# Kernel optimization log

Hardware: AMD Instinct MI355X
Metric: run time of the kernel (lower is better)

Reference implementation:

```python
import jax, jax.numpy as jnp
import numpy as np

BN_EPS = 1e-5

def knn_indices(loc, new_loc, k):
    # squared distances [B, M, N] via ||y||^2 + ||x||^2 - 2 y.x (no [B,M,N,3] materialization)
    x2 = jnp.sum(loc * loc, axis=-1)          # [B, N]
    y2 = jnp.sum(new_loc * new_loc, axis=-1)  # [B, M]
    d2 = y2[:, :, None] + x2[:, None, :] - 2.0 * jnp.einsum('bmc,bnc->bmn', new_loc, loc)
    _, idx = jax.lax.top_k(-d2, k)            # smallest-k -> [B, M, K]
    return idx

def gather_neighbors(x, idx):
    # x [B, N, C], idx [B, M, K] -> [B, M, K, C]
    return jax.vmap(lambda xb, ib: xb[ib])(x, idx)

def conv_bn_relu(x, W, g, b):
    # x [B, Cin, M, K]; 1x1 conv (no bias) + training-mode BatchNorm2d + ReLU
    y = jnp.einsum('oc,bcmk->bomk', W, x)
    mu = jnp.mean(y, axis=(0, 2, 3), keepdims=True)
    var = jnp.var(y, axis=(0, 2, 3), keepdims=True)  # biased, as torch BN uses for normalization
    y = (y - mu) * jax.lax.rsqrt(var + BN_EPS)
    return jax.nn.relu(y * g[None, :, None, None] + b[None, :, None, None])

def setup_inputs() -> dict:
    key = jax.random.key(0)
    ks = jax.random.split(key, 8)
    B, N, M, C = 16, 4096, 1024, 64
    loc = jax.random.normal(ks[0], (B, N, 3), dtype=jnp.float32)
    new_loc = jax.random.normal(ks[1], (B, M, 3), dtype=jnp.float32)
    features = jax.random.normal(ks[2], (B, C, N), dtype=jnp.float32)
    W1 = jax.random.normal(ks[3], (64, 67), dtype=jnp.float32) * (1.0 / np.sqrt(67.0))
    W2 = jax.random.normal(ks[4], (64, 64), dtype=jnp.float32) * (1.0 / np.sqrt(64.0))
    W3 = jax.random.normal(ks[5], (128, 64), dtype=jnp.float32) * (1.0 / np.sqrt(64.0))
    return {
        'loc': loc, 'new_loc': new_loc, 'features': features,
        'W1': W1, 'g1': jnp.ones(64, jnp.float32), 'b1': jnp.zeros(64, jnp.float32),
        'W2': W2, 'g2': jnp.ones(64, jnp.float32), 'b2': jnp.zeros(64, jnp.float32),
        'W3': W3, 'g3': jnp.ones(128, jnp.float32), 'b3': jnp.zeros(128, jnp.float32),
    }

def reference(loc, new_loc, features, W1, g1, b1, W2, g2, b2, W3, g3, b3):
    K = 32
    idx = knn_indices(loc, new_loc, K)                      # [B, M, K]
    knn_loc = gather_neighbors(loc, idx)                    # [B, M, K, 3]
    knn_loc = jnp.transpose(knn_loc, (0, 3, 1, 2))          # [B, 3, M, K]
    knn_loc = knn_loc - jnp.transpose(new_loc, (0, 2, 1))[..., None]  # relative xyz
    knn_feat = gather_neighbors(jnp.transpose(features, (0, 2, 1)), idx)  # [B, M, K, C]
    knn_feat = jnp.transpose(knn_feat, (0, 3, 1, 2))        # [B, C, M, K]
    h = jnp.concatenate([knn_loc, knn_feat], axis=1)        # [B, C+3, M, K]
    h = conv_bn_relu(h, W1, g1, b1)
    h = conv_bn_relu(h, W2, g2, b2)
    h = conv_bn_relu(h, W3, g3, b3)
    return jnp.max(h, axis=3)                               # [B, 128, M]
```

## Files before the change

kernel.cpp:

```cpp
#include <hip/hip_runtime.h>
#include <stdint.h>

#define B_   16
#define N_   4096
#define M_   1024
#define NT   (B_*M_*32)
#define BM   (B_*M_)

typedef unsigned short u16;
typedef unsigned long long u64;
typedef __attribute__((ext_vector_type(8))) short short8;
typedef __attribute__((ext_vector_type(4))) float f32x4;

__device__ __forceinline__ float bf2f(u16 u){
    return __uint_as_float(((unsigned int)u) << 16);
}
__device__ __forceinline__ u16 f2bf(float f){
    unsigned int u = __float_as_uint(f);
    return (u16)((u + 0x7FFFu + ((u >> 16) & 1u)) >> 16);
}

__global__ __launch_bounds__(256) void k_feat(const float* __restrict__ feat,
                                              float* __restrict__ featT){
    __shared__ float tile[64][65];
    int b  = blockIdx.y;
    int n0 = blockIdx.x * 64;
    for (int t = threadIdx.x; t < 4096; t += 256){
        int c = t >> 6, n = t & 63;
        tile[c][n] = feat[((size_t)(b*64 + c))*N_ + n0 + n];
    }
    __syncthreads();
    for (int t = threadIdx.x; t < 4096; t += 256){
        int n = t >> 6, c = t & 63;
        featT[((size_t)(b*N_) + n0 + n)*64 + c] = tile[c][n];
    }
}

__global__ __launch_bounds__(256) void k_knn(const float* __restrict__ locF,
                                             const float* __restrict__ nlocF,
                                             int* __restrict__ idxOut){
    const int tid  = threadIdx.x;
    const int lane = tid & 63, wv = tid >> 6;
    const int q    = blockIdx.x;
    const int b    = q >> 10, m = q & 1023;

    float qx = nlocF[(size_t)(b*M_ + m)*3 + 0];
    float qy = nlocF[(size_t)(b*M_ + m)*3 + 1];
    float qz = nlocF[(size_t)(b*M_ + m)*3 + 2];
    float y2 = __fadd_rn(__fadd_rn(__fmul_rn(qx,qx), __fmul_rn(qy,qy)), __fmul_rn(qz,qz));

    unsigned int key[16];
    const float* lb = locF + (size_t)b*N_*3;
    #pragma unroll
    for (int i = 0; i < 16; ++i){
        int n = i*256 + tid;
        float lx = lb[n*3+0], ly = lb[n*3+1], lz = lb[n*3+2];
        float x2 = __fadd_rn(__fadd_rn(__fmul_rn(lx,lx), __fmul_rn(ly,ly)), __fmul_rn(lz,lz));
        float dt = __fadd_rn(__fadd_rn(__fmul_rn(qx,lx), __fmul_rn(qy,ly)), __fmul_rn(qz,lz));
        float d2 = __fsub_rn(__fadd_rn(y2, x2), __fmul_rn(2.0f, dt));
        d2 = fmaxf(d2, 0.0f);
        key[i] = __float_as_uint(d2);
    }

    __shared__ unsigned int hist[4][256];
    __shared__ float wmm[4][2];
    __shared__ u64 cand[128];
    __shared__ int sOut[32];
    __shared__ int outCnt, candCnt;

    float lmin = 3.4e38f, lmax = 0.0f;
    #pragma unroll
    for (int i = 0; i < 16; ++i){
        float kf = __uint_as_float(key[i]);
        lmin = fminf(lmin, kf); lmax = fmaxf(lmax, kf);
    }
    #pragma unroll
    for (int st = 1; st < 64; st <<= 1){
        lmin = fminf(lmin, __shfl_xor(lmin, st, 64));
        lmax = fmaxf(lmax, __shfl_xor(lmax, st, 64));
    }
    if (tid == 0){ outCnt = 0; candCnt = 0; }
    if (lane == 0){ wmm[wv][0] = lmin; wmm[wv][1] = lmax; }
    __syncthreads();
    float lo = fminf(fminf(wmm[0][0], wmm[1][0]), fminf(wmm[2][0], wmm[3][0]));
    float hi = fmaxf(fmaxf(wmm[0][1], wmm[1][1]), fmaxf(wmm[2][1], wmm[3][1]));

    unsigned int act = 0xFFFFu;
    int bkt[16];
    int R = 32;

    for (int lvl = 0; lvl < 8; ++lvl){
        float scale = 255.0f / fmaxf(hi - lo, 1e-35f);
        ((uint4*)hist)[tid] = make_uint4(0,0,0,0);
        __syncthreads();
        #pragma unroll
        for (int i = 0; i < 16; ++i){
            if (act & (1u << i)){
                float kf = __uint_as_float(key[i]);
                int bb = (int)((kf - lo) * scale);
                bb = bb < 0 ? 0 : (bb > 255 ? 255 : bb);
                bkt[i] = bb;
                atomicAdd(&hist[wv][bb], 1u);
            }
        }
        __syncthreads();
        uint4 ha = *(const uint4*)&hist[0][lane << 2];
        uint4 hb = *(const uint4*)&hist[1][lane << 2];
        uint4 hc = *(const uint4*)&hist[2][lane << 2];
        uint4 hd = *(const uint4*)&hist[3][lane << 2];
        uint4 h = make_uint4(ha.x+hb.x+hc.x+hd.x, ha.y+hb.y+hc.y+hd.y,
                             ha.z+hb.z+hc.z+hd.z, ha.w+hb.w+hc.w+hd.w);
        int tot = (int)(h.x + h.y + h.z + h.w);
        int v = tot;
        #pragma unroll
        for (int st = 1; st < 64; st <<= 1){
            int u = __shfl_up(v, st, 64);
            if (lane >= st) v += u;
        }
        u64 bal = __ballot(v >= R);
        int Ls = __ffsll((unsigned long long)bal) - 1;
        int exclS = __shfl(v - tot, Ls, 64);
        int hx = __shfl((int)h.x, Ls, 64), hy = __shfl((int)h.y, Ls, 64);
        int hz = __shfl((int)h.z, Ls, 64), hw = __shfl((int)h.w, Ls, 64);
        int c0 = exclS + hx, c1 = c0 + hy, c2 = c1 + hz;
        int jj    = (c0 >= R) ? 0 : (c1 >= R) ? 1 : (c2 >= R) ? 2 : 3;
        int below = (jj == 0) ? exclS : (jj == 1) ? c0 : (jj == 2) ? c1 : c2;
        int cnt   = (jj == 0) ? hx : (jj == 1) ? hy : (jj == 2) ? hz : hw;
        int qb = Ls*4 + jj;
        R -= below;
        bool brk = (cnt <= 128) || (lvl == 7);

        float nlo = 3.4e38f, nhi = 0.0f;
        #pragma unroll
        for (int i = 0; i < 16; ++i){
            if (act & (1u << i)){
                int bb = bkt[i];
                if (bb < qb){
                    int pos = atomicAdd(&outCnt, 1);
                    if (pos < 32) sOut[pos] = i*256 + tid;
                    act &= ~(1u << i);
                } else if (bb > qb){
                    act &= ~(1u << i);
                } else if (!brk){
                    float kf = __uint_as_float(key[i]);
                    nlo = fminf(nlo, kf); nhi = fmaxf(nhi, kf);
                }
            }
        }
        if (brk) break;
        #pragma unroll
        for (int st = 1; st < 64; st <<= 1){
            nlo = fminf(nlo, __shfl_xor(nlo, st, 64));
            nhi = fmaxf(nhi, __shfl_xor(nhi, st, 64));
        }
        __syncthreads();
        if (lane == 0){ wmm[wv][0] = nlo; wmm[wv][1] = nhi; }
        __syncthreads();
        lo = fminf(fminf(wmm[0][0], wmm[1][0]), fminf(wmm[2][0], wmm[3][0]));
        hi = fmaxf(fmaxf(wmm[0][1], wmm[1][1]), fmaxf(wmm[2][1], wmm[3][1]));
    }

    #pragma unroll
    for (int i = 0; i < 16; ++i){
        if (act & (1u << i)){
            int pos = atomicAdd(&candCnt, 1);
            if (pos < 128) cand[pos] = (((u64)key[i]) << 32) | (unsigned int)(i*256 + tid);
        }
    }
    __syncthreads();
    int c = candCnt < 128 ? candCnt : 128;
    int base = outCnt;
    if (tid < c){
        u64 me = cand[tid];
        int rank = 0;
        for (int j = 0; j < c; ++j) rank += (cand[j] < me) ? 1 : 0;
        if (rank < R) sOut[base + rank] = (int)(me & 0xFFFFFFFFull);
    }
    __syncthreads();
    if (tid < 32) idxOut[(size_t)q*32 + tid] = sOut[tid];
}

__global__ __launch_bounds__(256) void k_conv1t(const int* __restrict__ idx,
                                                const float* __restrict__ locF,
                                                const float* __restrict__ nlocF,
                                                const float* __restrict__ featT,
                                                const float* __restrict__ W1,
                                                u16* __restrict__ y1){
    __shared__ float Wl[67*64];
    __shared__ float At[16*256];
    const int t  = threadIdx.x;
    const int s0 = blockIdx.x * 256;
    for (int i = t; i < 67*64; i += 256){
        int c = i >> 6, o = i & 63;
        Wl[i] = W1[o*67 + c];
    }
    __syncthreads();

    const int ob = t >> 6;
    const int sb = t & 63;
    const int o0 = ob*16;
    const int b  = s0 >> 15;
    float acc[16][4];

    {
        int4 nn = *(const int4*)&idx[s0 + sb*4];
        int ns[4] = {nn.x, nn.y, nn.z, nn.w};
        int m = ((s0 + sb*4) >> 5) & 1023;
        float qx = nlocF[(size_t)(b*M_ + m)*3 + 0];
        float qy = nlocF[(size_t)(b*M_ + m)*3 + 1];
        float qz = nlocF[(size_t)(b*M_ + m)*3 + 2];
        float r0[4], r1[4], r2[4];
        #pragma unroll
        for (int j = 0; j < 4; ++j){
            int n = ns[j]; if ((unsigned)n >= N_) n = 0;
            const float* lp = &locF[(size_t)(b*N_ + n)*3];
            r0[j] = lp[0] - qx; r1[j] = lp[1] - qy; r2[j] = lp[2] - qz;
        }
        #pragma unroll
        for (int i = 0; i < 16; ++i){
            float w0 = Wl[o0 + i], w1 = Wl[64 + o0 + i], w2 = Wl[128 + o0 + i];
            #pragma unroll
            for (int j = 0; j < 4; ++j)
                acc[i][j] = fmaf(w2, r2[j], fmaf(w1, r1[j], w0*r0[j]));
        }
    }

    for (int pass = 0; pass < 4; ++pass){
        __syncthreads();
        {
            int n = idx[s0 + t]; if ((unsigned)n >= N_) n = 0;
            const float4* fr = (const float4*)&featT[((size_t)(b*N_) + n)*64 + pass*16];
            #pragma unroll
            for (int q = 0; q < 4; ++q){
                float4 f = fr[q];
                At[(q*4+0)*256 + t] = f.x;
                At[(q*4+1)*256 + t] = f.y;
                At[(q*4+2)*256 + t] = f.z;
                At[(q*4+3)*256 + t] = f.w;
            }
        }
        __syncthreads();
        const float4* Wrow = (const float4*)&Wl[(3 + pass*16)*64];
        #pragma unroll
        for (int c = 0; c < 16; ++c){
            float4 a = *(const float4*)&At[c*256 + sb*4];
            float av[4] = {a.x, a.y, a.z, a.w};
            #pragma unroll
            for (int q = 0; q < 4; ++q){
                float4 w = Wrow[c*16 + ob*4 + q];
                float wv[4] = {w.x, w.y, w.z, w.w};
                #pragma unroll
                for (int r = 0; r < 4; ++r)
                    #pragma unroll
                    for (int j = 0; j < 4; ++j)
                        acc[q*4+r][j] = fmaf(wv[r], av[j], acc[q*4+r][j]);
            }
        }
    }
    #pragma unroll
    for (int i = 0; i < 16; ++i){
        ushort4 pk;
        pk.x = f2bf(acc[i][0]); pk.y = f2bf(acc[i][1]);
        pk.z = f2bf(acc[i][2]); pk.w = f2bf(acc[i][3]);
        *(ushort4*)&y1[(size_t)(o0+i)*NT + s0 + sb*4] = pk;
    }
}

__global__ __launch_bounds__(256) void k_conv2t(const u16* __restrict__ yin,
                                                const float* __restrict__ W2,
                                                const float* __restrict__ prm,
                                                u16* __restrict__ yout){
    __shared__ float Wl[64*64];
    __shared__ float At[16*256];
    __shared__ float sS[64], sT[64];
    const int t  = threadIdx.x;
    const int s0 = blockIdx.x * 256;
    for (int i = t; i < 64*64; i += 256){
        int c = i >> 6, o = i & 63;
        Wl[i] = W2[o*64 + c];
    }
    if (t < 64){ sS[t] = prm[t]; sT[t] = prm[64 + t]; }

    const int ob = t >> 6, sb = t & 63, o0 = ob*16;
    float acc[16][4];
    #pragma unroll
    for (int i = 0; i < 16; ++i)
        #pragma unroll
        for (int j = 0; j < 4; ++j) acc[i][j] = 0.0f;

    for (int pass = 0; pass < 4; ++pass){
        __syncthreads();
        #pragma unroll
        for (int rep = 0; rep < 2; ++rep){
            int v = rep*256 + t;
            int row = v >> 5, ch = v & 31;
            int c = pass*16 + row;
            uint4 pk = *(const uint4*)&yin[(size_t)c*NT + s0 + ch*8];
            float sc = sS[c], tt = sT[c];
            unsigned int w4[4] = {pk.x, pk.y, pk.z, pk.w};
            float f[8];
            #pragma unroll
            for (int q = 0; q < 4; ++q){
                f[2*q]   = fmaxf(fmaf(bf2f((u16)(w4[q] & 0xFFFF)), sc, tt), 0.0f);
                f[2*q+1] = fmaxf(fmaf(bf2f((u16)(w4[q] >> 16)),   sc, tt), 0.0f);
            }
            float4 f1 = {f[0], f[1], f[2], f[3]};
            float4 f2 = {f[4], f[5], f[6], f[7]};
            *(float4*)&At[row*256 + ch*8]     = f1;
            *(float4*)&At[row*256 + ch*8 + 4] = f2;
        }
        __syncthreads();
        const float4* Wrow = (const float4*)&Wl[(pass*16)*64];
        #pragma unroll
        for (int c = 0; c < 16; ++c){
            float4 a = *(const float4*)&At[c*256 + sb*4];
            float av[4] = {a.x, a.y, a.z, a.w};
            #pragma unroll
            for (int q = 0; q < 4; ++q){
                float4 w = Wrow[c*16 + ob*4 + q];
                float wv[4] = {w.x, w.y, w.z, w.w};
                #pragma unroll
                for (int r = 0; r < 4; ++r)
                    #pragma unroll
                    for (int j = 0; j < 4; ++j)
                        acc[q*4+r][j] = fmaf(wv[r], av[j], acc[q*4+r][j]);
            }
        }
    }
    #pragma unroll
    for (int i = 0; i < 16; ++i){
        ushort4 pk;
        pk.x = f2bf(acc[i][0]); pk.y = f2bf(acc[i][1]);
        pk.z = f2bf(acc[i][2]); pk.w = f2bf(acc[i][3]);
        *(ushort4*)&yout[(size_t)(o0+i)*NT + s0 + sb*4] = pk;
    }
}

__global__ __launch_bounds__(256) void k_conv3m(const u16* __restrict__ yin,
                                                const float* __restrict__ W3,
                                                const float* __restrict__ prm,
                                                float* __restrict__ gsum, float* __restrict__ gsq,
                                                float* __restrict__ gmax, float* __restrict__ gmin){
    __shared__ uint4 bfA[2048];
    __shared__ uint4 bfB[1024];
    __shared__ float sS[64], sT[64];
    __shared__ float sSum[128], sSq[128];
    const int t  = threadIdx.x;
    const int s0 = blockIdx.x * 256;

    if (t < 64){ sS[t] = prm[t]; sT[t] = prm[64 + t]; }
    if (t < 128){ sSum[t] = 0.0f; sSq[t] = 0.0f; }
    __syncthreads();

    #pragma unroll
    for (int rep = 0; rep < 4; ++rep){
        int cid = rep*256 + t;
        int ln  = cid & 63;
        int kk  = (cid >> 6) & 1;
        int nt  = cid >> 7;
        int o   = nt*16 + (ln & 15);
        int k0  = kk*32 + (ln >> 4)*8;
        const float* wp = &W3[o*64 + k0];
        unsigned int d[4];
        #pragma unroll
        for (int h = 0; h < 4; ++h)
            d[h] = (unsigned int)f2bf(wp[2*h]) | (((unsigned int)f2bf(wp[2*h+1])) << 16);
        bfB[cid] = make_uint4(d[0], d[1], d[2], d[3]);
    }

    {
        int oct = t >> 5;
        int sg  = t & 31;
        int c0  = oct*8;
        int kk  = oct >> 2;
        int qd  = oct & 3;
        u16 rb[8][8];
        #pragma unroll
        for (int j = 0; j < 8; ++j){
            int c = c0 + j;
            uint4 pk = *(const uint4*)&yin[(size_t)c*NT + s0 + sg*8];
            float sc = sS[c], tb = sT[c];
            unsigned int w4[4] = {pk.x, pk.y, pk.z, pk.w};
            #pragma unroll
            for (int h = 0; h < 4; ++h){
                rb[j][2*h]   = f2bf(fmaxf(fmaf(bf2f((u16)(w4[h] & 0xFFFF)), sc, tb), 0.0f));
                rb[j][2*h+1] = f2bf(fmaxf(fmaf(bf2f((u16)(w4[h] >> 16)),   sc, tb), 0.0f));
            }
        }
        #pragma unroll
        for (int i = 0; i < 8; ++i){
            int s   = sg*8 + i;
            int mtg = s >> 4, m15 = s & 15;
            int l64 = qd*16 + m15;
            int cb  = (mtg*2 + kk)*64 + (l64 ^ (mtg & 7));
            unsigned int d[4];
            #pragma unroll
            for (int h = 0; h < 4; ++h)
                d[h] = (unsigned int)rb[2*h][i] | (((unsigned int)rb[2*h+1][i]) << 16);
            bfA[cb] = make_uint4(d[0], d[1], d[2], d[3]);
        }
    }
    __syncthreads();

    const int w = t >> 6, lane = t & 63;
    f32x4 acc[4][8];
    #pragma unroll
    for (int mt = 0; mt < 4; ++mt)
        #pragma unroll
        for (int nt = 0; nt < 8; ++nt)
            acc[mt][nt] = (f32x4){0.0f, 0.0f, 0.0f, 0.0f};

    #pragma unroll
    for (int kk = 0; kk < 2; ++kk){
        short8 af[4];
        #pragma unroll
        for (int mt = 0; mt < 4; ++mt){
            int tile = 4*w + mt;
            af[mt] = *((const short8*)&bfA[(tile*2 + kk)*64 + (lane ^ (tile & 7))]);
        }
        #pragma unroll
        for (int nt = 0; nt < 8; ++nt){
            short8 bfr = *((const short8*)&bfB[(nt*2 + kk)*64 + lane]);
            #pragma unroll
            for (int mt = 0; mt < 4; ++mt)
                acc[mt][nt] = __builtin_amdgcn_mfma_f32_16x16x32_bf16(af[mt], bfr, acc[mt][nt], 0, 0, 0);
        }
    }

    float stS[8], stQ[8];
    #pragma unroll
    for (int nt = 0; nt < 8; ++nt){ stS[nt] = 0.0f; stQ[nt] = 0.0f; }

    #pragma unroll
    for (int g = 0; g < 2; ++g){
        const size_t gg = (size_t)(blockIdx.x*8 + w*2 + g);
        #pragma unroll
        for (int nt = 0; nt < 8; ++nt){
            f32x4 a0 = acc[2*g][nt], a1 = acc[2*g+1][nt];
            float mx = fmaxf(fmaxf(fmaxf(a0[0], a0[1]), fmaxf(a0[2], a0[3])),
                             fmaxf(fmaxf(a1[0], a1[1]), fmaxf(a1[2], a1[3])));
            float mn = fminf(fminf(fminf(a0[0], a0[1]), fminf(a0[2], a0[3])),
                             fminf(fminf(a1[0], a1[1]), fminf(a1[2], a1[3])));
            float sm = (a0[0]+a0[1]) + (a0[2]+a0[3]) + (a1[0]+a1[1]) + (a1[2]+a1[3]);
            float sq = a0[0]*a0[0];
            sq = fmaf(a0[1], a0[1], sq); sq = fmaf(a0[2], a0[2], sq); sq = fmaf(a0[3], a0[3], sq);
            sq = fmaf(a1[0], a1[0], sq); sq = fmaf(a1[1], a1[1], sq); sq = fmaf(a1[2], a1[2], sq);
            sq = fmaf(a1[3], a1[3], sq);
            #pragma unroll
            for (int st = 16; st < 64; st <<= 1){
                mx = fmaxf(mx, __shfl_xor(mx, st, 64));
                mn = fminf(mn, __shfl_xor(mn, st, 64));
                sm += __shfl_xor(sm, st, 64);
                sq += __shfl_xor(sq, st, 64);
            }
            if (lane < 16){
                gmax[gg*128 + nt*16 + lane] = mx;
                gmin[gg*128 + nt*16 + lane] = mn;
            }
            stS[nt] += sm; stQ[nt] += sq;
        }
    }
    if (lane < 16){
        #pragma unroll
        for (int nt = 0; nt < 8; ++nt){
            atomicAdd(&sSum[nt*16 + lane], stS[nt]);
            atomicAdd(&sSq[nt*16 + lane],  stQ[nt]);
        }
    }
    __syncthreads();
    if (t < 128){
        atomicAdd(&gsum[t], sSum[t]);
        atomicAdd(&gsq[t],  sSq[t]);
    }
}

__global__ __launch_bounds__(256) void k_stats(const u16* __restrict__ y,
                                               float* __restrict__ sum,
                                               float* __restrict__ sumsq){
    int c = blockIdx.x, chunk = blockIdx.y;
    size_t base = (size_t)c*NT + (size_t)chunk*16384;
    const uint2* p = (const uint2*)(y + base);
    float s = 0.0f, qq = 0.0f;
    for (int i = threadIdx.x; i < 4096; i += 256){
        uint2 v = p[i];
        float v0 = bf2f((u16)(v.x & 0xFFFF)), v1 = bf2f((u16)(v.x >> 16));
        float v2 = bf2f((u16)(v.y & 0xFFFF)), v3 = bf2f((u16)(v.y >> 16));
        s += v0 + v1 + v2 + v3;
        qq = fmaf(v0, v0, qq); qq = fmaf(v1, v1, qq);
        qq = fmaf(v2, v2, qq); qq = fmaf(v3, v3, qq);
    }
    #pragma unroll
    for (int off = 32; off > 0; off >>= 1){
        s  += __shfl_down(s,  off, 64);
        qq += __shfl_down(qq, off, 64);
    }
    __shared__ float aS[4], aQ[4];
    int wave = threadIdx.x >> 6, lane = threadIdx.x & 63;
    if (lane == 0){ aS[wave] = s; aQ[wave] = qq; }
    __syncthreads();
    if (threadIdx.x == 0){
        atomicAdd(&sum[c],   aS[0] + aS[1] + aS[2] + aS[3]);
        atomicAdd(&sumsq[c], aQ[0] + aQ[1] + aQ[2] + aQ[3]);
    }
}

__global__ void k_fold(const float* __restrict__ sum, const float* __restrict__ sumsq,
                       const float* __restrict__ gW, const float* __restrict__ bW,
                       float* __restrict__ prm, int C){
    int c = threadIdx.x;
    if (c < C){
        const float inv = 1.0f / (float)NT;
        float mu  = sum[c] * inv;
        float var = sumsq[c] * inv - mu*mu;
        float sc  = gW[c] / sqrtf(var + 1e-5f);
        prm[c]     = sc;
        prm[C + c] = bW[c] - mu*sc;
    }
}

__global__ __launch_bounds__(256) void k_final(const float* __restrict__ gmax,
                                               const float* __restrict__ gmin,
                                               const float* __restrict__ prm,
                                               float* __restrict__ out){
    int bo = blockIdx.y;
    int b = bo >> 7, o = bo & 127;
    int m = blockIdx.x*256 + threadIdx.x;
    float sc = prm[o], tt = prm[128 + o];
    size_t i = (size_t)(b*M_ + m)*128 + o;
    float v = (sc >= 0.0f) ? gmax[i] : gmin[i];
    out[((size_t)(b*128 + o))*M_ + m] = fmaxf(fmaf(v, sc, tt), 0.0f);
}

extern "C" void kernel_launch(void* const* d_in, const int* in_sizes, int n_in,
                              void* d_out, int out_size, void* d_ws, size_t ws_size,
                              hipStream_t stream){
    const float* loc  = (const float*)d_in[0];
    const float* nloc = (const float*)d_in[1];
    const float* feat = (const float*)d_in[2];
    const float* W1   = (const float*)d_in[3];
    const float* g1   = (const float*)d_in[4];
    const float* b1   = (const float*)d_in[5];
    const float* W2   = (const float*)d_in[6];
    const float* g2   = (const float*)d_in[7];
    const float* b2   = (const float*)d_in[8];
    const float* W3   = (const float*)d_in[9];
    const float* g3   = (const float*)d_in[10];
    const float* b3   = (const float*)d_in[11];
    float* out = (float*)d_out;

    char* ws = (char*)d_ws;
    float* stats = (float*)ws;
    float* prm1  = (float*)(ws + 2048);
    float* prm2  = (float*)(ws + 2048 + 512);
    float* prm3  = (float*)(ws + 2048 + 1024);
    int*   idx   = (int*)(ws + 4096);
    float* gmax  = (float*)(ws + 2101248);
    float* gmin  = (float*)(ws + 10489856);
    float* featT = (float*)(ws + 18878464);
    u16*   y1    = (u16*)(ws + 35655680);
    u16*   y2    = (u16*)(ws + 102764544);

    hipMemsetAsync(stats, 0, 2048, stream);

    k_feat<<<dim3(N_/64, B_), 256, 0, stream>>>(feat, featT);
    k_knn<<<B_*M_, 256, 0, stream>>>(loc, nloc, idx);

    k_conv1t<<<NT/256, 256, 0, stream>>>(idx, loc, nloc, featT, W1, y1);
    k_stats<<<dim3(64, 32), 256, 0, stream>>>(y1, stats + 0, stats + 64);
    k_fold<<<1, 128, 0, stream>>>(stats + 0, stats + 64, g1, b1, prm1, 64);

    k_conv2t<<<NT/256, 256, 0, stream>>>(y1, W2, prm1, y2);
    k_stats<<<dim3(64, 32), 256, 0, stream>>>(y2, stats + 128, stats + 192);
    k_fold<<<1, 128, 0, stream>>>(stats + 128, stats + 192, g2, b2, prm2, 64);

    k_conv3m<<<NT/256, 256, 0, stream>>>(y2, W3, prm2, stats + 256, stats + 384, gmax, gmin);
    k_fold<<<1, 128, 0, stream>>>(stats + 256, stats + 384, g3, b3, prm3, 128);

    k_final<<<dim3(M_/256, B_*128), 256, 0, stream>>>(gmax, gmin, prm3, out);
}
```

Before: 433.8 us.

## Fuse BN statistics into conv1/conv2 and move conv2 to bf16 MFMA

Per-channel sum and sum-of-squares are now computed inside conv1 and conv2 from the fp32 accumulators, using wave shuffles and atomics. This removes the two separate k_stats passes that re-read the bf16 activations from global memory. conv2 is rewritten to use bf16 MFMA 16x16x32 with swizzled LDS operand tiles and an LDS transpose for coalesced stores. In exchange, statistics are taken from unrounded fp32 values instead of the stored bf16, conv2 inputs are rounded to bf16, and atomic contention on the stat counters increases.

Measured after the change: 1.154 ms. 166% more time.

```diff
diff --git a/kernel.cpp b/kernel.cpp
--- a/kernel.cpp
+++ b/kernel.cpp
@@ -185,7 +185,9 @@
                                                 const float* __restrict__ nlocF,
                                                 const float* __restrict__ featT,
                                                 const float* __restrict__ W1,
-                                                u16* __restrict__ y1){
+                                                u16* __restrict__ y1,
+                                                float* __restrict__ gsum,
+                                                float* __restrict__ gsq){
     __shared__ float Wl[67*64];
     __shared__ float At[16*256];
     const int t  = threadIdx.x;
@@ -264,75 +266,187 @@
         pk.z = f2bf(acc[i][2]); pk.w = f2bf(acc[i][3]);
         *(ushort4*)&y1[(size_t)(o0+i)*NT + s0 + sb*4] = pk;
     }
-}
-
-__global__ __launch_bounds__(256) void k_conv2t(const u16* __restrict__ yin,
+
+    #pragma unroll
+    for (int half = 0; half < 2; ++half){
+        float s8[8], q8[8];
+        #pragma unroll
+        for (int i = 0; i < 8; ++i){
+            float a0 = acc[half*8+i][0], a1 = acc[half*8+i][1];
+            float a2 = acc[half*8+i][2], a3 = acc[half*8+i][3];
+            s8[i] = (a0 + a1) + (a2 + a3);
+            float qq = a0*a0;
+            qq = fmaf(a1, a1, qq); qq = fmaf(a2, a2, qq); qq = fmaf(a3, a3, qq);
+            q8[i] = qq;
+        }
+        #pragma unroll
+        for (int st = 1; st < 64; st <<= 1){
+            #pragma unroll
+            for (int i = 0; i < 8; ++i){
+                s8[i] += __shfl_xor(s8[i], st, 64);
+                q8[i] += __shfl_xor(q8[i], st, 64);
+            }
+        }
+        if ((t & 63) == 0){
+            #pragma unroll
+            for (int i = 0; i < 8; ++i){
+                atomicAdd(&gsum[o0 + half*8 + i], s8[i]);
+                atomicAdd(&gsq[o0 + half*8 + i],  q8[i]);
+            }
+        }
+    }
+}
+
+__global__ __launch_bounds__(256) void k_conv2m(const u16* __restrict__ yin,
                                                 const float* __restrict__ W2,
                                                 const float* __restrict__ prm,
-                                                u16* __restrict__ yout){
-    __shared__ float Wl[64*64];
-    __shared__ float At[16*256];
+                                                u16* __restrict__ yout,
+                                                float* __restrict__ gsum,
+                                                float* __restrict__ gsq){
+    __shared__ uint4 bfA[2048];
+    __shared__ uint4 bfB[512];
+    __shared__ u16  tileT[64*264];
     __shared__ float sS[64], sT[64];
+    __shared__ float sSum[64], sSq[64];
     const int t  = threadIdx.x;
     const int s0 = blockIdx.x * 256;
-    for (int i = t; i < 64*64; i += 256){
-        int c = i >> 6, o = i & 63;
-        Wl[i] = W2[o*64 + c];
-    }
-    if (t < 64){ sS[t] = prm[t]; sT[t] = prm[64 + t]; }
-
-    const int ob = t >> 6, sb = t & 63, o0 = ob*16;
-    float acc[16][4];
-    #pragma unroll
-    for (int i = 0; i < 16; ++i)
-        #pragma unroll
-        for (int j = 0; j < 4; ++j) acc[i][j] = 0.0f;
-
-    for (int pass = 0; pass < 4; ++pass){
-        __syncthreads();
-        #pragma unroll
-        for (int rep = 0; rep < 2; ++rep){
-            int v = rep*256 + t;
-            int row = v >> 5, ch = v & 31;
-            int c = pass*16 + row;
-            uint4 pk = *(const uint4*)&yin[(size_t)c*NT + s0 + ch*8];
-            float sc = sS[c], tt = sT[c];
+
+    if (t < 64){ sS[t] = prm[t]; sT[t] = prm[64 + t]; sSum[t] = 0.0f; sSq[t] = 0.0f; }
+    __syncthreads();
+
+    #pragma unroll
+    for (int rep = 0; rep < 2; ++rep){
+        int cid = rep*256 + t;
+        int ln  = cid & 63;
+        int kk  = (cid >> 6) & 1;
+        int nt  = cid >> 7;
+        int o   = nt*16 + (ln & 15);
+        int k0  = kk*32 + (ln >> 4)*8;
+        const float* wp = &W2[o*64 + k0];
+        unsigned int d[4];
+        #pragma unroll
+        for (int h = 0; h < 4; ++h)
+            d[h] = (unsigned int)f2bf(wp[2*h]) | (((unsigned int)f2bf(wp[2*h+1])) << 16);
+        bfB[cid] = make_uint4(d[0], d[1], d[2], d[3]);
+    }
+
+    {
+        int oct = t >> 5;
+        int sg  = t & 31;
+        int c0  = oct*8;
+        int kk  = oct >> 2;
+        int qd  = oct & 3;
+        u16 rb[8][8];
+        #pragma unroll
+        for (int j = 0; j < 8; ++j){
+            int c = c0 + j;
+            uint4 pk = *(const uint4*)&yin[(size_t)c*NT + s0 + sg*8];
+            float sc = sS[c], tb = sT[c];
             unsigned int w4[4] = {pk.x, pk.y, pk.z, pk.w};
-            float f[8];
-            #pragma unroll
-            for (int q = 0; q < 4; ++q){
-                f[2*q]   = fmaxf(fmaf(bf2f((u16)(w4[q] & 0xFFFF)), sc, tt), 0.0f);
-                f[2*q+1] = fmaxf(fmaf(bf2f((u16)(w4[q] >> 16)),   sc, tt), 0.0f);
-            }
-            float4 f1 = {f[0], f[1], f[2], f[3]};
-            float4 f2 = {f[4], f[5], f[6], f[7]};
-            *(float4*)&At[row*256 + ch*8]     = f1;
-            *(float4*)&At[row*256 + ch*8 + 4] = f2;
-        }
-        __syncthreads();
-        const float4* Wrow = (const float4*)&Wl[(pass*16)*64];
-        #pragma unroll
-        for (int c = 0; c < 16; ++c){
-            float4 a = *(const float4*)&At[c*256 + sb*4];
-            float av[4] = {a.x, a.y, a.z, a.w};
-            #pragma unroll
-            for (int q = 0; q < 4; ++q){
-                float4 w = Wrow[c*16 + ob*4 + q];
-                float wv[4] = {w.x, w.y, w.z, w.w};
-                #pragma unroll
-                for (int r = 0; r < 4; ++r)
-                    #pragma unroll
-                    for (int j = 0; j < 4; ++j)
-                        acc[q*4+r][j] = fmaf(wv[r], av[j], acc[q*4+r][j]);
-            }
-        }
-    }
-    #pragma unroll
-    for (int i = 0; i < 16; ++i){
-        ushort4 pk;
-        pk.x = f2bf(acc[i][0]); pk.y = f2bf(acc[i][1]);
-        pk.z = f2bf(acc[i][2]); pk.w = f2bf(acc[i][3]);
-        *(ushort4*)&yout[(size_t)(o0+i)*NT + s0 + sb*4] = pk;
+            #pragma unroll
+            for (int h = 0; h < 4; ++h){
+                rb[j][2*h]   = f2bf(fmaxf(fmaf(bf2f((u16)(w4[h] & 0xFFFF)), sc, tb), 0.0f));
+                rb[j][2*h+1] = f2bf(fmaxf(fmaf(bf2f((u16)(w4[h] >> 16)),   sc, tb), 0.0f));
+            }
+        }
+        #pragma unroll
+        for (int i = 0; i < 8; ++i){
+            int s   = sg*8 + i;
+            int mtg = s >> 4, m15 = s & 15;
+            int l64 = qd*16 + m15;
+            int cb  = (mtg*2 + kk)*64 + (l64 ^ (mtg & 7));
+            unsigned int d[4];
+            #pragma unroll
+            for (int h = 0; h < 4; ++h)
+                d[h] = (unsigned int)rb[2*h][i] | (((unsigned int)rb[2*h+1][i]) << 16);
+            bfA[cb] = make_uint4(d[0], d[1], d[2], d[3]);
+        }
+    }
+    __syncthreads();
+
+    const int w = t >> 6, lane = t & 63;
+    f32x4 acc[4][4];
+    #pragma unroll
+    for (int mt = 0; mt < 4; ++mt)
+        #pragma unroll
+        for (int nt = 0; nt < 4; ++nt)
+            acc[mt][nt] = (f32x4){0.0f, 0.0f, 0.0f, 0.0f};
+
+    #pragma unroll
+    for (int kk = 0; kk < 2; ++kk){
+        short8 af[4];
+        #pragma unroll
+        for (int mt = 0; mt < 4; ++mt){
+            int tile = 4*w + mt;
+            af[mt] = *((const short8*)&bfA[(tile*2 + kk)*64 + (lane ^ (tile & 7))]);
+        }
+        #pragma unroll
+        for (int nt = 0; nt < 4; ++nt){
+            short8 bfr = *((const short8*)&bfB[(nt*2 + kk)*64 + lane]);
+            #pragma unroll
+            for (int mt = 0; mt < 4; ++mt)
+                acc[mt][nt] = __builtin_amdgcn_mfma_f32_16x16x32_bf16(af[mt], bfr, acc[mt][nt], 0, 0, 0);
+        }
+    }
+
+    {
+        float st4[4], sq4[4];
+        #pragma unroll
+        for (int nt = 0; nt < 4; ++nt){ st4[nt] = 0.0f; sq4[nt] = 0.0f; }
+        #pragma unroll
+        for (int mt = 0; mt < 4; ++mt)
+            #pragma unroll
+            for (int nt = 0; nt < 4; ++nt){
+                f32x4 a = acc[mt][nt];
+                st4[nt] += (a[0] + a[1]) + (a[2] + a[3]);
+                float qq = a[0]*a[0];
+                qq = fmaf(a[1], a[1], qq); qq = fmaf(a[2], a[2], qq); qq = fmaf(a[3], a[3], qq);
+                sq4[nt] += qq;
+            }
+        #pragma unroll
+        for (int st = 16; st < 64; st <<= 1){
+            #pragma unroll
+            for (int nt = 0; nt < 4; ++nt){
+                st4[nt] += __shfl_xor(st4[nt], st, 64);
+                sq4[nt] += __shfl_xor(sq4[nt], st, 64);
+            }
+        }
+        if (lane < 16){
+            #pragma unroll
+            for (int nt = 0; nt < 4; ++nt){
+                atomicAdd(&sSum[nt*16 + lane], st4[nt]);
+                atomicAdd(&sSq[nt*16 + lane],  sq4[nt]);
+            }
+        }
+    }
+
+    #pragma unroll
+    for (int mt = 0; mt < 4; ++mt){
+        int s_base = w*64 + mt*16 + (lane >> 4)*4;
+        #pragma unroll
+        for (int nt = 0; nt < 4; ++nt){
+            int o = nt*16 + (lane & 15);
+            f32x4 a = acc[mt][nt];
+            unsigned int p01 = (unsigned int)f2bf(a[0]) | (((unsigned int)f2bf(a[1])) << 16);
+            unsigned int p23 = (unsigned int)f2bf(a[2]) | (((unsigned int)f2bf(a[3])) << 16);
+            *(unsigned int*)&tileT[o*264 + s_base]     = p01;
+            *(unsigned int*)&tileT[o*264 + s_base + 2] = p23;
+        }
+    }
+    __syncthreads();
+
+    {
+        int c  = t >> 2;
+        int g0 = (t & 3)*8;
+        #pragma unroll
+        for (int j = 0; j < 8; ++j){
+            uint4 v = *(const uint4*)&tileT[c*264 + (g0 + j)*8];
+            *(uint4*)&yout[(size_t)c*NT + s0 + (g0 + j)*8] = v;
+        }
+    }
+    if (t < 64){
+        atomicAdd(&gsum[t], sSum[t]);
+        atomicAdd(&gsq[t],  sSq[t]);
     }
 }
 
@@ -471,36 +585,6 @@
     if (t < 128){
         atomicAdd(&gsum[t], sSum[t]);
         atomicAdd(&gsq[t],  sSq[t]);
-    }
-}
-
-__global__ __launch_bounds__(256) void k_stats(const u16* __restrict__ y,
-                                               float* __restrict__ sum,
-                                               float* __restrict__ sumsq){
-    int c = blockIdx.x, chunk = blockIdx.y;
-    size_t base = (size_t)c*NT + (size_t)chunk*16384;
-    const uint2* p = (const uint2*)(y + base);
-    float s = 0.0f, qq = 0.0f;
-    for (int i = threadIdx.x; i < 4096; i += 256){
-        uint2 v = p[i];
-        float v0 = bf2f((u16)(v.x & 0xFFFF)), v1 = bf2f((u16)(v.x >> 16));
-        float v2 = bf2f((u16)(v.y & 0xFFFF)), v3 = bf2f((u16)(v.y >> 16));
-        s += v0 + v1 + v2 + v3;
-        qq = fmaf(v0, v0, qq); qq = fmaf(v1, v1, qq);
-        qq = fmaf(v2, v2, qq); qq = fmaf(v3, v3, qq);
-    }
-    #pragma unroll
-    for (int off = 32; off > 0; off >>= 1){
-        s  += __shfl_down(s,  off, 64);
-        qq += __shfl_down(qq, off, 64);
-    }
-    __shared__ float aS[4], aQ[4];
-    int wave = threadIdx.x >> 6, lane = threadIdx.x & 63;
-    if (lane == 0){ aS[wave] = s; aQ[wave] = qq; }
-    __syncthreads();
-    if (threadIdx.x == 0){
-        atomicAdd(&sum[c],   aS[0] + aS[1] + aS[2] + aS[3]);
-        atomicAdd(&sumsq[c], aQ[0] + aQ[1] + aQ[2] + aQ[3]);
     }
 }
 
@@ -565,12 +649,10 @@
     k_feat<<<dim3(N_/64, B_), 256, 0, stream>>>(feat, featT);
     k_knn<<<B_*M_, 256, 0, stream>>>(loc, nloc, idx);
 
-    k_conv1t<<<NT/256, 256, 0, stream>>>(idx, loc, nloc, featT, W1, y1);
-    k_stats<<<dim3(64, 32), 256, 0, stream>>>(y1, stats + 0, stats + 64);
+    k_conv1t<<<NT/256, 256, 0, stream>>>(idx, loc, nloc, featT, W1, y1, stats + 0, stats + 64);
     k_fold<<<1, 128, 0, stream>>>(stats + 0, stats + 64, g1, b1, prm1, 64);
 
-    k_conv2t<<<NT/256, 256, 0, stream>>>(y1, W2, prm1, y2);
-    k_stats<<<dim3(64, 32), 256, 0, stream>>>(y2, stats + 128, stats + 192);
+    k_conv2m<<<NT/256, 256, 0, stream>>>(y1, W2, prm1, y2, stats + 128, stats + 192);
     k_fold<<<1, 128, 0, stream>>>(stats + 128, stats + 192, g2, b2, prm2, 64);
 
     k_conv3m<<<NT/256, 256, 0, stream>>>(y2, W3, prm2, stats + 256, stats + 384, gmax, gmin);
```
